# Kernel tuning notes

Hardware: AMD Instinct MI355X
Metric: run time of the kernel (lower is better)

Reference implementation:

```python
import jax, jax.numpy as jnp
import numpy as np

H = 64
VOCAB = 128
LN_EPS = 1e-5
NORM_EPS = 1e-12


def _l2norm(k):
    # F.normalize(..., dim=-1): x / max(||x||_2, eps)
    n = jnp.sqrt(jnp.sum(k * k, axis=-1, keepdims=True))
    return k / jnp.maximum(n, NORM_EPS)


def _delta_scan(M0, ks, vs):
    # ks, vs: [L, B, H] time-major; M0: [B, H, H]
    def step(M, kv):
        k, v = kv
        Mk = jnp.einsum('bij,bj->bi', M, k)            # [B,H]
        M = M + (v - Mk)[:, :, None] * k[:, None, :]   # rank-1 update
        return M, None
    M, _ = jax.lax.scan(step, M0, (ks, vs))
    return M


def reference(x, embed, W1, b1, W2, b2, ln_g, ln_b, Wk, Wv, Wq, Wattn, Wout, bout):
    # Encoder: embed -> residual FF -> LayerNorm
    h = embed[x]                                        # [B,L,H]
    ff = jnp.maximum(h @ W1.T + b1, 0.0) @ W2.T + b2
    z = h + ff
    mu = jnp.mean(z, axis=-1, keepdims=True)
    var = jnp.mean((z - mu) ** 2, axis=-1, keepdims=True)
    hidden = (z - mu) / jnp.sqrt(var + LN_EPS) * ln_g + ln_b  # [B,L,H]

    B, L, _ = hidden.shape
    # First delta-rule memory write over all L steps
    ks = _l2norm(hidden @ Wk.T)                         # [B,L,H]
    vs = hidden @ Wv.T                                  # [B,L,H]
    M0 = jnp.zeros((B, H, H), dtype=hidden.dtype)
    M = _delta_scan(M0, jnp.swapaxes(ks, 0, 1), jnp.swapaxes(vs, 0, 1))

    half = L // 2
    slots = jnp.swapaxes(M, 1, 2)                       # [B,H,H] = M^T
    q = hidden[:, :half, :] @ Wattn.T                   # [B,half,H]
    # bmm(q, slots^T) = q @ M
    attn = jax.nn.softmax(jnp.einsum('bth,bhk->btk', q, M) / jnp.sqrt(jnp.asarray(H, hidden.dtype)), axis=-1)
    ctx = jnp.einsum('btk,bkh->bth', attn, slots)       # [B,half,H]

    # Second delta-rule write seeded from M
    ks2 = _l2norm(ctx @ Wk.T)
    vs2 = ctx @ Wv.T
    M2 = _delta_scan(M, jnp.swapaxes(ks2, 0, 1), jnp.swapaxes(vs2, 0, 1))

    q_last = hidden[:, -1, :] @ Wq.T                    # [B,H]
    read = jnp.einsum('bij,bj->bi', M2, q_last)         # [B,H]
    return read @ Wout.T + bout                         # [B,VOCAB]


def setup_inputs() -> dict:
    key = jax.random.key(0)
    ks = jax.random.split(key, 16)
    B, L = 64, 4096
    s = 0.05
    return {
        'x': jax.random.randint(ks[0], (B, L), 0, VOCAB),
        'embed': jax.random.normal(ks[1], (VOCAB, H), jnp.float32) * s,
        'W1': jax.random.normal(ks[2], (2 * H, H), jnp.float32) * s,
        'b1': jnp.zeros((2 * H,), jnp.float32),
        'W2': jax.random.normal(ks[3], (H, 2 * H), jnp.float32) * s,
        'b2': jnp.zeros((H,), jnp.float32),
        'ln_g': jnp.ones((H,), jnp.float32),
        'ln_b': jnp.zeros((H,), jnp.float32),
        'Wk': jax.random.normal(ks[4], (H, H), jnp.float32) * s,
        'Wv': jax.random.normal(ks[5], (H, H), jnp.float32) * s,
        'Wq': jax.random.normal(ks[6], (H, H), jnp.float32) * s,
        'Wattn': jax.random.normal(ks[7], (H, H), jnp.float32) * s,
        'Wout': jax.random.normal(ks[8], (VOCAB, H), jnp.float32) * s,
        'bout': jnp.zeros((VOCAB,), jnp.float32),
    }
```

## Files before the change

### kernel.cpp

```cpp
#include <hip/hip_runtime.h>

#define SEQL 4096
#define NB 64

__device__ __forceinline__ float dpp_xor1_add(float x) {
    int v = __builtin_amdgcn_mov_dpp(__float_as_int(x), 0xB1, 0xF, 0xF, true);
    return x + __int_as_float(v);
}
__device__ __forceinline__ float dpp_xor2_add(float x) {
    int v = __builtin_amdgcn_mov_dpp(__float_as_int(x), 0x4E, 0xF, 0xF, true);
    return x + __int_as_float(v);
}

#define FMA16(A, W, H)                                      \
    A[0]  = fmaf(W.x, H.x, A[0]);  A[1]  = fmaf(W.x, H.y, A[1]);   \
    A[2]  = fmaf(W.x, H.z, A[2]);  A[3]  = fmaf(W.x, H.w, A[3]);   \
    A[4]  = fmaf(W.y, H.x, A[4]);  A[5]  = fmaf(W.y, H.y, A[5]);   \
    A[6]  = fmaf(W.y, H.z, A[6]);  A[7]  = fmaf(W.y, H.w, A[7]);   \
    A[8]  = fmaf(W.z, H.x, A[8]);  A[9]  = fmaf(W.z, H.y, A[9]);   \
    A[10] = fmaf(W.z, H.z, A[10]); A[11] = fmaf(W.z, H.w, A[11]);  \
    A[12] = fmaf(W.w, H.x, A[12]); A[13] = fmaf(W.w, H.y, A[13]);  \
    A[14] = fmaf(W.w, H.z, A[14]); A[15] = fmaf(W.w, H.w, A[15])

__device__ __forceinline__ void proj_tile64(const float* __restrict__ sW,
                                            const float* __restrict__ sA,
                                            int jq, int tq, float* __restrict__ a)
{
#pragma unroll
    for (int u = 0; u < 16; ++u) a[u] = 0.f;
#pragma unroll 4
    for (int i = 0; i < 64; ++i) {
        float4 w  = *reinterpret_cast<const float4*>(&sW[i * 68 + jq]);
        float4 h4 = *reinterpret_cast<const float4*>(&sA[i * 68 + tq]);
        FMA16(a, w, h4);
    }
}

__device__ __forceinline__ void load_w_t(const float* __restrict__ W, int ldw, int col0,
                                         int tid, float4* __restrict__ r)
{
    const int j = tid & 63;
    const int cq0 = tid >> 6;
#pragma unroll
    for (int it = 0; it < 4; ++it)
        r[it] = *reinterpret_cast<const float4*>(&W[(size_t)j * ldw + col0 + (it * 4 + cq0) * 4]);
}
__device__ __forceinline__ void write_w_t(const float4* __restrict__ r,
                                          float* __restrict__ sWb, int tid)
{
    const int j = tid & 63;
    const int cq0 = tid >> 6;
#pragma unroll
    for (int it = 0; it < 4; ++it) {
        const int c = (it * 4 + cq0) * 4;
        sWb[(c + 0) * 68 + j] = r[it].x;
        sWb[(c + 1) * 68 + j] = r[it].y;
        sWb[(c + 2) * 68 + j] = r[it].z;
        sWb[(c + 3) * 68 + j] = r[it].w;
    }
}

__device__ __forceinline__ void stage_w_t(const float* __restrict__ W, int ldw, int col0,
                                          float* __restrict__ sWb, int tid)
{
    float4 r[4];
    load_w_t(W, ldw, col0, tid, r);
    write_w_t(r, sWb, tid);
}
__device__ __forceinline__ void stage_w_n(const float* __restrict__ W,
                                          float* __restrict__ sWb, int tid)
{
#pragma unroll
    for (int it = 0; it < 4; ++it) {
        int item = it * 256 + tid;
        int r = item >> 4, c4 = item & 15;
        float4 w = *reinterpret_cast<const float4*>(&W[(size_t)r * 64 + c4 * 4]);
        *reinterpret_cast<float4*>(&sWb[r * 68 + c4 * 4]) = w;
    }
}

__global__ __launch_bounds__(256) void encoder_kernel(
    const int* __restrict__ x, const float* __restrict__ embed,
    const float* __restrict__ W1, const float* __restrict__ b1,
    const float* __restrict__ W2, const float* __restrict__ b2,
    const float* __restrict__ ln_g, const float* __restrict__ ln_b,
    const float* __restrict__ Wk, const float* __restrict__ Wv,
    const float* __restrict__ Wq, const float* __restrict__ Wattn,
    float* __restrict__ ks, float* __restrict__ vs,
    float* __restrict__ qbuf, float* __restrict__ qlast)
{
    __shared__ __align__(16) float sZ[64 * 68];
    __shared__ __align__(16) float sF[64 * 68];
    __shared__ __align__(16) float sW[64 * 68];

    const int tid = threadIdx.x;
    const size_t g0 = (size_t)blockIdx.x * 64;
    const int b = (int)(g0 >> 12);
    const int l0 = (int)(g0 & (SEQL - 1));
    const int jq = (tid & 15) * 4;
    const int tq = (tid >> 4) * 4;
    const bool doq = (l0 < 2048);
    const bool dolast = (l0 == SEQL - 64);

    float4 pf[4], pf2[4];

    load_w_t(W1, 64, 0, tid, pf);
    for (int idx = tid; idx < 4096; idx += 256) {
        int t = idx >> 6, i = idx & 63;
        sZ[i * 68 + t] = embed[(size_t)x[g0 + t] * 64 + i];
    }
    write_w_t(pf, sW, tid);
    load_w_t(W2, 128, 0, tid, pf2);
    __syncthreads();

    float zacc[16];
#pragma unroll
    for (int u = 0; u < 16; ++u) zacc[u] = 0.f;

    {
        float a[16];
        proj_tile64(sW, sZ, jq, tq, a);
        float4 bb = *reinterpret_cast<const float4*>(&b1[jq]);
        float bv[4] = {bb.x, bb.y, bb.z, bb.w};
#pragma unroll
        for (int u = 0; u < 4; ++u) {
            float4 o;
            o.x = fmaxf(a[u * 4 + 0] + bv[u], 0.f);
            o.y = fmaxf(a[u * 4 + 1] + bv[u], 0.f);
            o.z = fmaxf(a[u * 4 + 2] + bv[u], 0.f);
            o.w = fmaxf(a[u * 4 + 3] + bv[u], 0.f);
            *reinterpret_cast<float4*>(&sF[(jq + u) * 68 + tq]) = o;
        }
    }
    __syncthreads();
    write_w_t(pf2, sW, tid);
    load_w_t(W1 + 4096, 64, 0, tid, pf);
    __syncthreads();
#pragma unroll 4
    for (int p = 0; p < 64; ++p) {
        float4 w  = *reinterpret_cast<const float4*>(&sW[p * 68 + jq]);
        float4 f4 = *reinterpret_cast<const float4*>(&sF[p * 68 + tq]);
        FMA16(zacc, w, f4);
    }
    __syncthreads();
    write_w_t(pf, sW, tid);
    load_w_t(W2, 128, 64, tid, pf2);
    __syncthreads();
    {
        float a[16];
        proj_tile64(sW, sZ, jq, tq, a);
        float4 bb = *reinterpret_cast<const float4*>(&b1[64 + jq]);
        float bv[4] = {bb.x, bb.y, bb.z, bb.w};
#pragma unroll
        for (int u = 0; u < 4; ++u) {
            float4 o;
            o.x = fmaxf(a[u * 4 + 0] + bv[u], 0.f);
            o.y = fmaxf(a[u * 4 + 1] + bv[u], 0.f);
            o.z = fmaxf(a[u * 4 + 2] + bv[u], 0.f);
            o.w = fmaxf(a[u * 4 + 3] + bv[u], 0.f);
            *reinterpret_cast<float4*>(&sF[(jq + u) * 68 + tq]) = o;
        }
    }
    __syncthreads();
    write_w_t(pf2, sW, tid);
    load_w_t(Wk, 64, 0, tid, pf);
    load_w_t(Wv, 64, 0, tid, pf2);
    __syncthreads();
#pragma unroll 4
    for (int p = 0; p < 64; ++p) {
        float4 w  = *reinterpret_cast<const float4*>(&sW[p * 68 + jq]);
        float4 f4 = *reinterpret_cast<const float4*>(&sF[p * 68 + tq]);
        FMA16(zacc, w, f4);
    }

    {
        float z[16];
        float4 b2v = *reinterpret_cast<const float4*>(&b2[jq]);
        float bv[4] = {b2v.x, b2v.y, b2v.z, b2v.w};
#pragma unroll
        for (int u = 0; u < 4; ++u) {
            float4 h4 = *reinterpret_cast<const float4*>(&sZ[(jq + u) * 68 + tq]);
            z[u * 4 + 0] = h4.x + bv[u] + zacc[u * 4 + 0];
            z[u * 4 + 1] = h4.y + bv[u] + zacc[u * 4 + 1];
            z[u * 4 + 2] = h4.z + bv[u] + zacc[u * 4 + 2];
            z[u * 4 + 3] = h4.w + bv[u] + zacc[u * 4 + 3];
        }
        float s[4], ss[4];
#pragma unroll
        for (int v = 0; v < 4; ++v) {
            s[v]  = z[v] + z[4 + v] + z[8 + v] + z[12 + v];
            ss[v] = z[v] * z[v] + z[4 + v] * z[4 + v]
                  + z[8 + v] * z[8 + v] + z[12 + v] * z[12 + v];
        }
#pragma unroll
        for (int m = 1; m <= 8; m <<= 1) {
#pragma unroll
            for (int v = 0; v < 4; ++v) {
                s[v]  += __shfl_xor(s[v], m);
                ss[v] += __shfl_xor(ss[v], m);
            }
        }
        float mu[4], inv[4];
#pragma unroll
        for (int v = 0; v < 4; ++v) {
            mu[v] = s[v] * 0.015625f;
            float var = ss[v] * 0.015625f - mu[v] * mu[v];
            inv[v] = rsqrtf(var + 1e-5f);
        }
        float4 g4  = *reinterpret_cast<const float4*>(&ln_g[jq]);
        float4 be4 = *reinterpret_cast<const float4*>(&ln_b[jq]);
        float gv[4] = {g4.x, g4.y, g4.z, g4.w};
        float bev[4] = {be4.x, be4.y, be4.z, be4.w};
#pragma unroll
        for (int u = 0; u < 4; ++u) {
            float4 o;
            o.x = (z[u * 4 + 0] - mu[0]) * inv[0] * gv[u] + bev[u];
            o.y = (z[u * 4 + 1] - mu[1]) * inv[1] * gv[u] + bev[u];
            o.z = (z[u * 4 + 2] - mu[2]) * inv[2] * gv[u] + bev[u];
            o.w = (z[u * 4 + 3] - mu[3]) * inv[3] * gv[u] + bev[u];
            *reinterpret_cast<float4*>(&sZ[(jq + u) * 68 + tq]) = o;
        }
    }
    __syncthreads();
    write_w_t(pf, sW, tid);
    write_w_t(pf2, sF, tid);
    if (doq)        load_w_t(Wattn, 64, 0, tid, pf);
    else if (dolast) load_w_t(Wq, 64, 0, tid, pf);
    __syncthreads();

    {
        float a[16];
        proj_tile64(sW, sZ, jq, tq, a);
        float ssq[4];
#pragma unroll
        for (int v = 0; v < 4; ++v)
            ssq[v] = a[v] * a[v] + a[4 + v] * a[4 + v]
                   + a[8 + v] * a[8 + v] + a[12 + v] * a[12 + v];
#pragma unroll
        for (int m = 1; m <= 8; m <<= 1) {
#pragma unroll
            for (int v = 0; v < 4; ++v) ssq[v] += __shfl_xor(ssq[v], m);
        }
#pragma unroll
        for (int v = 0; v < 4; ++v) {
            float sc = 1.f / fmaxf(sqrtf(ssq[v]), 1e-12f);
            float4 o = make_float4(a[v] * sc, a[4 + v] * sc, a[8 + v] * sc, a[12 + v] * sc);
            *reinterpret_cast<float4*>(&ks[(g0 + tq + v) * 64 + jq]) = o;
        }
    }
    {
        float a[16];
        proj_tile64(sF, sZ, jq, tq, a);
#pragma unroll
        for (int v = 0; v < 4; ++v) {
            float4 o = make_float4(a[v], a[4 + v], a[8 + v], a[12 + v]);
            *reinterpret_cast<float4*>(&vs[(g0 + tq + v) * 64 + jq]) = o;
        }
    }

    if (doq || dolast) {
        __syncthreads();
        write_w_t(pf, sW, tid);
        __syncthreads();
        float a[16];
        proj_tile64(sW, sZ, jq, tq, a);
        if (doq) {
#pragma unroll
            for (int v = 0; v < 4; ++v) {
                float4 o = make_float4(a[v], a[4 + v], a[8 + v], a[12 + v]);
                *reinterpret_cast<float4*>(&qbuf[((size_t)b * 2048 + l0 + tq + v) * 64 + jq]) = o;
            }
        } else if ((tid >> 4) == 15) {
            float4 o = make_float4(a[3], a[7], a[11], a[15]);
            *reinterpret_cast<float4*>(&qlast[(size_t)b * 64 + jq]) = o;
        }
    }
}

#define STEP2(K0, K1, K2, K3, V)                                                \
    do {                                                                        \
        float dp0 = fmaf(p[0], K0.x, fmaf(p[1], K0.y, fmaf(p[2], K0.z, p[3] * K0.w))); \
        float dp1 = fmaf(p[4], K1.x, fmaf(p[5], K1.y, fmaf(p[6], K1.z, p[7] * K1.w))); \
        float dp2 = fmaf(p[8], K2.x, fmaf(p[9], K2.y, fmaf(p[10], K2.z, p[11] * K2.w))); \
        float dp3 = fmaf(p[12], K3.x, fmaf(p[13], K3.y, fmaf(p[14], K3.z, p[15] * K3.w))); \
        float dq0 = fmaf(q[0], K0.x, fmaf(q[1], K0.y, fmaf(q[2], K0.z, q[3] * K0.w))); \
        float dq1 = fmaf(q[4], K1.x, fmaf(q[5], K1.y, fmaf(q[6], K1.z, q[7] * K1.w))); \
        float dq2 = fmaf(q[8], K2.x, fmaf(q[9], K2.y, fmaf(q[10], K2.z, q[11] * K2.w))); \
        float dq3 = fmaf(q[12], K3.x, fmaf(q[13], K3.y, fmaf(q[14], K3.z, q[15] * K3.w))); \
        float ddp = (dp0 + dp1) + (dp2 + dp3);                                  \
        float ddq = (dq0 + dq1) + (dq2 + dq3);                                  \
        ddp = dpp_xor1_add(ddp);  ddq = dpp_xor1_add(ddq);                      \
        ddp = dpp_xor2_add(ddp);  ddq = dpp_xor2_add(ddq);                      \
        float up = -ddp;                                                        \
        float uq = V - ddq;                                                     \
        p[0] = fmaf(up, K0.x, p[0]);   q[0] = fmaf(uq, K0.x, q[0]);             \
        p[1] = fmaf(up, K0.y, p[1]);   q[1] = fmaf(uq, K0.y, q[1]);             \
        p[2] = fmaf(up, K0.z, p[2]);   q[2] = fmaf(uq, K0.z, q[2]);             \
        p[3] = fmaf(up, K0.w, p[3]);   q[3] = fmaf(uq, K0.w, q[3]);             \
        p[4] = fmaf(up, K1.x, p[4]);   q[4] = fmaf(uq, K1.x, q[4]);             \
        p[5] = fmaf(up, K1.y, p[5]);   q[5] = fmaf(uq, K1.y, q[5]);             \
        p[6] = fmaf(up, K1.z, p[6]);   q[6] = fmaf(uq, K1.z, q[6]);             \
        p[7] = fmaf(up, K1.w, p[7]);   q[7] = fmaf(uq, K1.w, q[7]);             \
        p[8] = fmaf(up, K2.x, p[8]);   q[8] = fmaf(uq, K2.x, q[8]);             \
        p[9] = fmaf(up, K2.y, p[9]);   q[9] = fmaf(uq, K2.y, q[9]);             \
        p[10] = fmaf(up, K2.z, p[10]); q[10] = fmaf(uq, K2.z, q[10]);           \
        p[11] = fmaf(up, K2.w, p[11]); q[11] = fmaf(uq, K2.w, q[11]);           \
        p[12] = fmaf(up, K3.x, p[12]); q[12] = fmaf(uq, K3.x, q[12]);           \
        p[13] = fmaf(up, K3.y, p[13]); q[13] = fmaf(uq, K3.y, q[13]);           \
        p[14] = fmaf(up, K3.z, p[14]); q[14] = fmaf(uq, K3.z, q[14]);           \
        p[15] = fmaf(up, K3.w, p[15]); q[15] = fmaf(uq, K3.w, q[15]);           \
    } while (0)

__global__ __launch_bounds__(256) void chunk_kernel(
    float* __restrict__ ksb, float* __restrict__ vsb, int C)
{
    __shared__ __align__(16) float sk[2][32 * 64];
    __shared__ __align__(16) float sv[2][32 * 64];

    const int job = blockIdx.x;
    const int tid = threadIdx.x;
    const int r = tid >> 2;
    const int c0 = (tid & 3) * 16;
    float* kc = ksb + (size_t)job * C * 64;
    float* vc = vsb + (size_t)job * C * 64;

    float p[16], q[16];
#pragma unroll
    for (int j = 0; j < 16; ++j) { p[j] = (c0 + j == r) ? 1.f : 0.f; q[j] = 0.f; }

    const int nt = C >> 5;
    float4 rk0, rk1, rv0, rv1;

    {
        const float4* gk = reinterpret_cast<const float4*>(kc);
        const float4* gv = reinterpret_cast<const float4*>(vc);
        float4 a0 = gk[tid], a1 = gk[256 + tid];
        float4 b0 = gv[tid], b1 = gv[256 + tid];
        float4* dk = reinterpret_cast<float4*>(sk[0]);
        float4* dv = reinterpret_cast<float4*>(sv[0]);
        dk[tid] = a0; dk[256 + tid] = a1;
        dv[tid] = b0; dv[256 + tid] = b1;
    }
    if (nt > 1) {
        const float4* gk = reinterpret_cast<const float4*>(kc + 2048);
        const float4* gv = reinterpret_cast<const float4*>(vc + 2048);
        rk0 = gk[tid]; rk1 = gk[256 + tid];
        rv0 = gv[tid]; rv1 = gv[256 + tid];
    }
    __syncthreads();

    int cur = 0;
    for (int tile = 0; tile < nt; ++tile) {
        if (tile + 1 < nt) {
            float4* dk = reinterpret_cast<float4*>(sk[cur ^ 1]);
            float4* dv = reinterpret_cast<float4*>(sv[cur ^ 1]);
            dk[tid] = rk0; dk[256 + tid] = rk1;
            dv[tid] = rv0; dv[256 + tid] = rv1;
            if (tile + 2 < nt) {
                const float4* gk = reinterpret_cast<const float4*>(kc + (size_t)(tile + 2) * 2048);
                const float4* gv = reinterpret_cast<const float4*>(vc + (size_t)(tile + 2) * 2048);
                rk0 = gk[tid]; rk1 = gk[256 + tid];
                rv0 = gv[tid]; rv1 = gv[256 + tid];
            }
        }

        const float* kl = sk[cur] + c0;
        const float* vl = sv[cur] + r;
        float4 a0, a1, a2, a3, e0, e1, e2, e3;
        float va, ve;
        {
            const float4* kp = reinterpret_cast<const float4*>(kl);
            a0 = kp[0]; a1 = kp[1]; a2 = kp[2]; a3 = kp[3];
            va = vl[0];
        }
#pragma unroll
        for (int t = 0; t < 32; t += 2) {
            {
                const float4* kp = reinterpret_cast<const float4*>(kl + (t + 1) * 64);
                e0 = kp[0]; e1 = kp[1]; e2 = kp[2]; e3 = kp[3];
                ve = vl[(t + 1) * 64];
            }
            STEP2(a0, a1, a2, a3, va);
            if (t + 2 < 32) {
                const float4* kp = reinterpret_cast<const float4*>(kl + (t + 2) * 64);
                a0 = kp[0]; a1 = kp[1]; a2 = kp[2]; a3 = kp[3];
                va = vl[(t + 2) * 64];
            }
            STEP2(e0, e1, e2, e3, ve);
        }
        __syncthreads();
        cur ^= 1;
    }

    float4* po = reinterpret_cast<float4*>(kc + r * 64 + c0);
    po[0] = make_float4(p[0], p[1], p[2], p[3]);
    po[1] = make_float4(p[4], p[5], p[6], p[7]);
    po[2] = make_float4(p[8], p[9], p[10], p[11]);
    po[3] = make_float4(p[12], p[13], p[14], p[15]);
    float4* qo = reinterpret_cast<float4*>(vc + r * 64 + c0);
    qo[0] = make_float4(q[0], q[1], q[2], q[3]);
    qo[1] = make_float4(q[4], q[5], q[6], q[7]);
    qo[2] = make_float4(q[8], q[9], q[10], q[11]);
    qo[3] = make_float4(q[12], q[13], q[14], q[15]);
}

__global__ __launch_bounds__(256) void combine_kernel(
    const float* __restrict__ Pb, const float* __restrict__ Qb,
    const float* __restrict__ Min, float* __restrict__ Mout,
    int nc, int chunk_stride)
{
    __shared__ __align__(16) float sP[2][64 * 64];
    __shared__ __align__(16) float sM[2][16 * 68];
    const int bb = blockIdx.x;
    const int b = bb >> 2;
    const int r0 = (bb & 3) << 4;
    const int tid = threadIdx.x;
    const int rl = tid >> 4;
    const int j4 = (tid & 15) * 4;
    const int gr = r0 + rl;

    if (Min) {
        *reinterpret_cast<float4*>(&sM[0][rl * 68 + j4]) =
            *reinterpret_cast<const float4*>(Min + ((size_t)b * 64 + gr) * 64 + j4);
    } else {
        *reinterpret_cast<float4*>(&sM[0][rl * 68 + j4]) = make_float4(0.f, 0.f, 0.f, 0.f);
    }
    {
        const float4* g = reinterpret_cast<const float4*>(Pb + (size_t)b * nc * chunk_stride);
        float4* s = reinterpret_cast<float4*>(sP[0]);
        for (int i = tid; i < 1024; i += 256) s[i] = g[i];
    }
    __syncthreads();

    int cur = 0;
    for (int c = 0; c < nc; ++c) {
        const size_t cbase = (size_t)(b * nc + c) * chunk_stride;
        float4 rp0, rp1, rp2, rp3;
        if (c + 1 < nc) {
            const float4* g = reinterpret_cast<const float4*>(Pb + cbase + chunk_stride);
            rp0 = g[tid]; rp1 = g[tid + 256]; rp2 = g[tid + 512]; rp3 = g[tid + 768];
        }
        float4 rq = *reinterpret_cast<const float4*>(Qb + cbase + (size_t)gr * 64 + j4);

        float ax = 0.f, ay = 0.f, az = 0.f, aw = 0.f;
        const float* Mrow = &sM[cur][rl * 68];
        const float* Pl = sP[c & 1];
#pragma unroll 4
        for (int mg = 0; mg < 16; ++mg) {
            float4 a4 = *reinterpret_cast<const float4*>(Mrow + mg * 4);
            float4 p0 = *reinterpret_cast<const float4*>(Pl + (mg * 4 + 0) * 64 + j4);
            float4 p1 = *reinterpret_cast<const float4*>(Pl + (mg * 4 + 1) * 64 + j4);
            float4 p2 = *reinterpret_cast<const float4*>(Pl + (mg * 4 + 2) * 64 + j4);
            float4 p3 = *reinterpret_cast<const float4*>(Pl + (mg * 4 + 3) * 64 + j4);
            ax = fmaf(a4.x, p0.x, ax); ay = fmaf(a4.x, p0.y, ay);
            az = fmaf(a4.x, p0.z, az); aw = fmaf(a4.x, p0.w, aw);
            ax = fmaf(a4.y, p1.x, ax); ay = fmaf(a4.y, p1.y, ay);
            az = fmaf(a4.y, p1.z, az); aw = fmaf(a4.y, p1.w, aw);
            ax = fmaf(a4.z, p2.x, ax); ay = fmaf(a4.z, p2.y, ay);
            az = fmaf(a4.z, p2.z, az); aw = fmaf(a4.z, p2.w, aw);
            ax = fmaf(a4.w, p3.x, ax); ay = fmaf(a4.w, p3.y, ay);
            az = fmaf(a4.w, p3.z, az); aw = fmaf(a4.w, p3.w, aw);
        }
        const int nxt = cur ^ 1;
        *reinterpret_cast<float4*>(&sM[nxt][rl * 68 + j4]) =
            make_float4(ax + rq.x, ay + rq.y, az + rq.z, aw + rq.w);
        if (c + 1 < nc) {
            float4* s = reinterpret_cast<float4*>(sP[(c + 1) & 1]);
            s[tid] = rp0; s[tid + 256] = rp1; s[tid + 512] = rp2; s[tid + 768] = rp3;
        }
        __syncthreads();
        cur = nxt;
    }
    *reinterpret_cast<float4*>(Mout + ((size_t)b * 64 + gr) * 64 + j4) =
        *reinterpret_cast<const float4*>(&sM[cur][rl * 68 + j4]);
}

__global__ __launch_bounds__(256) void attn_kernel(
    const float* __restrict__ qg, const float* __restrict__ Mbuf,
    const float* __restrict__ Wk, const float* __restrict__ Wv,
    float* __restrict__ ks2, float* __restrict__ vs2)
{
    __shared__ __align__(16) float sW1[64 * 68];
    __shared__ __align__(16) float sW2[64 * 68];
    __shared__ __align__(16) float sA[64 * 68];
    __shared__ __align__(16) float sB[64 * 68];

    const int b = blockIdx.y;
    const int tile0 = blockIdx.x * 64;
    const int tid = threadIdx.x;
    const int jq = (tid & 15) * 4;
    const int tq = (tid >> 4) * 4;
    const size_t qbase = (size_t)b * 2048 + tile0;
    const float* Mb = Mbuf + (size_t)b * 4096;

    stage_w_n(Mb, sW1, tid);
    stage_w_t(Mb, 64, 0, sW2, tid);
    stage_w_t(qg + qbase * 64, 64, 0, sA, tid);
    __syncthreads();

    float a[16];
    proj_tile64(sW1, sA, jq, tq, a);
#pragma unroll
    for (int u = 0; u < 16; ++u) a[u] *= 0.125f;

    {
        float mx[4], sm[4];
#pragma unroll
        for (int v = 0; v < 4; ++v)
            mx[v] = fmaxf(fmaxf(a[v], a[4 + v]), fmaxf(a[8 + v], a[12 + v]));
#pragma unroll
        for (int m = 1; m <= 8; m <<= 1) {
#pragma unroll
            for (int v = 0; v < 4; ++v) mx[v] = fmaxf(mx[v], __shfl_xor(mx[v], m));
        }
#pragma unroll
        for (int v = 0; v < 4; ++v) {
            a[v]      = __expf(a[v]      - mx[v]);
            a[4 + v]  = __expf(a[4 + v]  - mx[v]);
            a[8 + v]  = __expf(a[8 + v]  - mx[v]);
            a[12 + v] = __expf(a[12 + v] - mx[v]);
            sm[v] = a[v] + a[4 + v] + a[8 + v] + a[12 + v];
        }
#pragma unroll
        for (int m = 1; m <= 8; m <<= 1) {
#pragma unroll
            for (int v = 0; v < 4; ++v) sm[v] += __shfl_xor(sm[v], m);
        }
        float rinv[4];
#pragma unroll
        for (int v = 0; v < 4; ++v) rinv[v] = 1.f / sm[v];
#pragma unroll
        for (int v = 0; v < 4; ++v) {
            a[v] *= rinv[v]; a[4 + v] *= rinv[v];
            a[8 + v] *= rinv[v]; a[12 + v] *= rinv[v];
        }
    }
#pragma unroll
    for (int u = 0; u < 4; ++u)
        *reinterpret_cast<float4*>(&sB[(jq + u) * 68 + tq]) =
            make_float4(a[u * 4 + 0], a[u * 4 + 1], a[u * 4 + 2], a[u * 4 + 3]);
    __syncthreads();

    float c[16];
    proj_tile64(sW2, sB, jq, tq, c);
#pragma unroll
    for (int u = 0; u < 4; ++u)
        *reinterpret_cast<float4*>(&sA[(jq + u) * 68 + tq]) =
            make_float4(c[u * 4 + 0], c[u * 4 + 1], c[u * 4 + 2], c[u * 4 + 3]);
    __syncthreads();

    stage_w_t(Wk, 64, 0, sW1, tid);
    stage_w_t(Wv, 64, 0, sW2, tid);
    __syncthreads();

    float ak[16], av[16];
#pragma unroll
    for (int u = 0; u < 16; ++u) { ak[u] = 0.f; av[u] = 0.f; }
#pragma unroll 2
    for (int i = 0; i < 64; ++i) {
        float4 wk = *reinterpret_cast<const float4*>(&sW1[i * 68 + jq]);
        float4 wv = *reinterpret_cast<const float4*>(&sW2[i * 68 + jq]);
        float4 c4 = *reinterpret_cast<const float4*>(&sA[i * 68 + tq]);
        FMA16(ak, wk, c4);
        FMA16(av, wv, c4);
    }

    {
        float ssq[4];
#pragma unroll
        for (int v = 0; v < 4; ++v)
            ssq[v] = ak[v] * ak[v] + ak[4 + v] * ak[4 + v]
                   + ak[8 + v] * ak[8 + v] + ak[12 + v] * ak[12 + v];
#pragma unroll
        for (int m = 1; m <= 8; m <<= 1) {
#pragma unroll
            for (int v = 0; v < 4; ++v) ssq[v] += __shfl_xor(ssq[v], m);
        }
#pragma unroll
        for (int v = 0; v < 4; ++v) {
            float sc = 1.f / fmaxf(sqrtf(ssq[v]), 1e-12f);
            const size_t o = (qbase + tq + v) * 64 + jq;
            *reinterpret_cast<float4*>(&ks2[o]) =
                make_float4(ak[v] * sc, ak[4 + v] * sc, ak[8 + v] * sc, ak[12 + v] * sc);
            *reinterpret_cast<float4*>(&vs2[o]) =
                make_float4(av[v], av[4 + v], av[8 + v], av[12 + v]);
        }
    }
}

__global__ __launch_bounds__(128) void out_kernel(
    const float* __restrict__ M2, const float* __restrict__ qlast,
    const float* __restrict__ Wout, const float* __restrict__ bout,
    float* __restrict__ out)
{
    const int b = blockIdx.x;
    const int tid = threadIdx.x;
    __shared__ float sq[64], sread[64];
    if (tid < 64) sq[tid] = qlast[b * 64 + tid];
    __syncthreads();
    if (tid < 64) {
        const float* Mr = M2 + ((size_t)b * 64 + tid) * 64;
        float acc = 0.f;
        for (int j = 0; j < 64; ++j) acc = fmaf(Mr[j], sq[j], acc);
        sread[tid] = acc;
    }
    __syncthreads();
    float acc = bout[tid];
    for (int h = 0; h < 64; ++h) acc = fmaf(Wout[tid * 64 + h], sread[h], acc);
    out[b * 128 + tid] = acc;
}

extern "C" void kernel_launch(void* const* d_in, const int* in_sizes, int n_in,
                              void* d_out, int out_size, void* d_ws, size_t ws_size,
                              hipStream_t stream)
{
    const int* x        = (const int*)d_in[0];
    const float* embed  = (const float*)d_in[1];
    const float* W1     = (const float*)d_in[2];
    const float* b1     = (const float*)d_in[3];
    const float* W2     = (const float*)d_in[4];
    const float* b2     = (const float*)d_in[5];
    const float* ln_g   = (const float*)d_in[6];
    const float* ln_b   = (const float*)d_in[7];
    const float* Wk     = (const float*)d_in[8];
    const float* Wv     = (const float*)d_in[9];
    const float* Wq     = (const float*)d_in[10];
    const float* Wattn  = (const float*)d_in[11];
    const float* Wout   = (const float*)d_in[12];
    const float* bout   = (const float*)d_in[13];

    float* ws = (float*)d_ws;
    float* ks = ws;
    float* vs = ks + (size_t)NB * SEQL * 64;
    float* qb = vs + (size_t)NB * SEQL * 64;
    float* ql = qb + (size_t)NB * 2048 * 64;
    float* M  = ql + (size_t)NB * 64;
    float* M2 = M + (size_t)NB * 64 * 64;
    if (ws_size < (size_t)(M2 + (size_t)NB * 64 * 64 - ws) * sizeof(float)) return;

    hipLaunchKernelGGL(encoder_kernel, dim3((NB * SEQL) / 64), dim3(256), 0, stream,
                       x, embed, W1, b1, W2, b2, ln_g, ln_b, Wk, Wv, Wq, Wattn,
                       ks, vs, qb, ql);

    const int C1 = 256, nc1 = SEQL / C1;
    hipLaunchKernelGGL(chunk_kernel, dim3(NB * nc1), dim3(256), 0, stream, ks, vs, C1);
    hipLaunchKernelGGL(combine_kernel, dim3(NB * 4), dim3(256), 0, stream,
                       ks, vs, (const float*)nullptr, M, nc1, C1 * 64);

    hipLaunchKernelGGL(attn_kernel, dim3(32, NB), dim3(256), 0, stream,
                       qb, M, Wk, Wv, ks, vs);

    const int C2 = 128, nc2 = 2048 / C2;
    hipLaunchKernelGGL(chunk_kernel, dim3(NB * nc2), dim3(256), 0, stream, ks, vs, C2);
    hipLaunchKernelGGL(combine_kernel, dim3(NB * 4), dim3(256), 0, stream,
                       ks, vs, M, M2, nc2, C2 * 64);

    hipLaunchKernelGGL(out_kernel, dim3(NB), dim3(128), 0, stream,
                       M2, ql, Wout, bout, (float*)d_out);
}
```

Baseline: 494.6 us.

## Fold Wattn, Wk, Wv into per-batch memory matrices before attention

A new per-batch precompute kernel forms Wattn-times-M, M-times-Wk^T and M-times-Wv^T once, so the attention kernel reads the hidden states directly instead of a separately projected q buffer. The encoder now writes the first half of the hidden states transposed instead of computing the Wattn projection. The attention kernel drops one 64x64 matmul stage per tile along with its shared buffer and barrier, and prefetches MK through registers. In exchange it adds a small extra launch and roughly 64K extra floats of workspace reads, and it changes the floating-point association order.

```diff
diff --git a/kernel.cpp b/kernel.cpp
--- a/kernel.cpp
+++ b/kernel.cpp
@@ -85,9 +85,9 @@
     const float* __restrict__ W2, const float* __restrict__ b2,
     const float* __restrict__ ln_g, const float* __restrict__ ln_b,
     const float* __restrict__ Wk, const float* __restrict__ Wv,
-    const float* __restrict__ Wq, const float* __restrict__ Wattn,
+    const float* __restrict__ Wq,
     float* __restrict__ ks, float* __restrict__ vs,
-    float* __restrict__ qbuf, float* __restrict__ qlast)
+    float* __restrict__ hidT, float* __restrict__ qlast)
 {
     __shared__ __align__(16) float sZ[64 * 68];
     __shared__ __align__(16) float sF[64 * 68];
@@ -224,8 +224,7 @@
     __syncthreads();
     write_w_t(pf, sW, tid);
     write_w_t(pf2, sF, tid);
-    if (doq)        load_w_t(Wattn, 64, 0, tid, pf);
-    else if (dolast) load_w_t(Wq, 64, 0, tid, pf);
+    if (dolast) load_w_t(Wq, 64, 0, tid, pf);
     __syncthreads();
 
     {
@@ -258,22 +257,74 @@
         }
     }
 
-    if (doq || dolast) {
+    if (doq) {
+#pragma unroll
+        for (int it = 0; it < 4; ++it) {
+            int item = it * 256 + tid;
+            int i = item >> 4, q4 = (item & 15) * 4;
+            float4 v = *reinterpret_cast<const float4*>(&sZ[i * 68 + q4]);
+            *reinterpret_cast<float4*>(&hidT[((size_t)b * 64 + i) * 2048 + l0 + q4]) = v;
+        }
+    }
+
+    if (dolast) {
         __syncthreads();
         write_w_t(pf, sW, tid);
         __syncthreads();
         float a[16];
         proj_tile64(sW, sZ, jq, tq, a);
-        if (doq) {
-#pragma unroll
-            for (int v = 0; v < 4; ++v) {
-                float4 o = make_float4(a[v], a[4 + v], a[8 + v], a[12 + v]);
-                *reinterpret_cast<float4*>(&qbuf[((size_t)b * 2048 + l0 + tq + v) * 64 + jq]) = o;
-            }
-        } else if ((tid >> 4) == 15) {
+        if ((tid >> 4) == 15) {
             float4 o = make_float4(a[3], a[7], a[11], a[15]);
             *reinterpret_cast<float4*>(&qlast[(size_t)b * 64 + jq]) = o;
         }
+    }
+}
+
+__global__ __launch_bounds__(256) void precompute_kernel(
+    const float* __restrict__ Mbuf, const float* __restrict__ Wattn,
+    const float* __restrict__ Wk, const float* __restrict__ Wv,
+    float* __restrict__ WAM, float* __restrict__ MK, float* __restrict__ MV)
+{
+    __shared__ __align__(16) float sM[64 * 68];
+    __shared__ __align__(16) float sOp[64 * 68];
+    const int b = blockIdx.x;
+    const int tid = threadIdx.x;
+    const int jq = (tid & 15) * 4;
+    const int tq = (tid >> 4) * 4;
+    const float* Mb = Mbuf + (size_t)b * 4096;
+
+    stage_w_n(Mb, sM, tid);
+    stage_w_n(Wattn, sOp, tid);
+    __syncthreads();
+    {
+        float a[16];
+        proj_tile64(sM, sOp, jq, tq, a);
+#pragma unroll
+        for (int v = 0; v < 4; ++v)
+            *reinterpret_cast<float4*>(&WAM[(size_t)b * 4096 + (tq + v) * 64 + jq]) =
+                make_float4(a[v], a[4 + v], a[8 + v], a[12 + v]);
+    }
+    __syncthreads();
+    stage_w_t(Wk, 64, 0, sOp, tid);
+    __syncthreads();
+    {
+        float a[16];
+        proj_tile64(sM, sOp, jq, tq, a);
+#pragma unroll
+        for (int v = 0; v < 4; ++v)
+            *reinterpret_cast<float4*>(&MK[(size_t)b * 4096 + (tq + v) * 64 + jq]) =
+                make_float4(a[v], a[4 + v], a[8 + v], a[12 + v]);
+    }
+    __syncthreads();
+    stage_w_t(Wv, 64, 0, sOp, tid);
+    __syncthreads();
+    {
+        float a[16];
+        proj_tile64(sM, sOp, jq, tq, a);
+#pragma unroll
+        for (int v = 0; v < 4; ++v)
+            *reinterpret_cast<float4*>(&MV[(size_t)b * 4096 + (tq + v) * 64 + jq]) =
+                make_float4(a[v], a[4 + v], a[8 + v], a[12 + v]);
     }
 }
 
@@ -476,14 +527,13 @@
 }
 
 __global__ __launch_bounds__(256) void attn_kernel(
-    const float* __restrict__ qg, const float* __restrict__ Mbuf,
-    const float* __restrict__ Wk, const float* __restrict__ Wv,
+    const float* __restrict__ hidT, const float* __restrict__ WAM,
+    const float* __restrict__ MK, const float* __restrict__ MV,
     float* __restrict__ ks2, float* __restrict__ vs2)
 {
     __shared__ __align__(16) float sW1[64 * 68];
     __shared__ __align__(16) float sW2[64 * 68];
     __shared__ __align__(16) float sA[64 * 68];
-    __shared__ __align__(16) float sB[64 * 68];
 
     const int b = blockIdx.y;
     const int tile0 = blockIdx.x * 64;
@@ -491,11 +541,19 @@
     const int jq = (tid & 15) * 4;
     const int tq = (tid >> 4) * 4;
     const size_t qbase = (size_t)b * 2048 + tile0;
-    const float* Mb = Mbuf + (size_t)b * 4096;
-
-    stage_w_n(Mb, sW1, tid);
-    stage_w_t(Mb, 64, 0, sW2, tid);
-    stage_w_t(qg + qbase * 64, 64, 0, sA, tid);
+    const float* hb = hidT + (size_t)b * 64 * 2048 + tile0;
+
+    float4 pfk[4];
+    stage_w_n(WAM + (size_t)b * 4096, sW1, tid);
+    stage_w_t(MV + (size_t)b * 4096, 64, 0, sW2, tid);
+#pragma unroll
+    for (int it = 0; it < 4; ++it) {
+        int item = it * 256 + tid;
+        int i = item >> 4, q4 = (item & 15) * 4;
+        float4 v = *reinterpret_cast<const float4*>(&hb[(size_t)i * 2048 + q4]);
+        *reinterpret_cast<float4*>(&sA[i * 68 + q4]) = v;
+    }
+    load_w_t(MK + (size_t)b * 4096, 64, 0, tid, pfk);
     __syncthreads();
 
     float a[16];
@@ -535,22 +593,12 @@
             a[8 + v] *= rinv[v]; a[12 + v] *= rinv[v];
         }
     }
-#pragma unroll
-    for (int u = 0; u < 4; ++u)
-        *reinterpret_cast<float4*>(&sB[(jq + u) * 68 + tq]) =
-            make_float4(a[u * 4 + 0], a[u * 4 + 1], a[u * 4 + 2], a[u * 4 + 3]);
-    __syncthreads();
-
-    float c[16];
-    proj_tile64(sW2, sB, jq, tq, c);
+    __syncthreads();
 #pragma unroll
     for (int u = 0; u < 4; ++u)
         *reinterpret_cast<float4*>(&sA[(jq + u) * 68 + tq]) =
-            make_float4(c[u * 4 + 0], c[u * 4 + 1], c[u * 4 + 2], c[u * 4 + 3]);
-    __syncthreads();
-
-    stage_w_t(Wk, 64, 0, sW1, tid);
-    stage_w_t(Wv, 64, 0, sW2, tid);
+            make_float4(a[u * 4 + 0], a[u * 4 + 1], a[u * 4 + 2], a[u * 4 + 3]);
+    write_w_t(pfk, sW1, tid);
     __syncthreads();
 
     float ak[16], av[16];
@@ -560,9 +608,9 @@
     for (int i = 0; i < 64; ++i) {
         float4 wk = *reinterpret_cast<const float4*>(&sW1[i * 68 + jq]);
         float4 wv = *reinterpret_cast<const float4*>(&sW2[i * 68 + jq]);
-        float4 c4 = *reinterpret_cast<const float4*>(&sA[i * 68 + tq]);
-        FMA16(ak, wk, c4);
-        FMA16(av, wv, c4);
+        float4 p4 = *reinterpret_cast<const float4*>(&sA[i * 68 + tq]);
+        FMA16(ak, wk, p4);
+        FMA16(av, wv, p4);
     }
 
     {
@@ -630,25 +678,31 @@
     const float* bout   = (const float*)d_in[13];
 
     float* ws = (float*)d_ws;
-    float* ks = ws;
-    float* vs = ks + (size_t)NB * SEQL * 64;
-    float* qb = vs + (size_t)NB * SEQL * 64;
-    float* ql = qb + (size_t)NB * 2048 * 64;
-    float* M  = ql + (size_t)NB * 64;
-    float* M2 = M + (size_t)NB * 64 * 64;
-    if (ws_size < (size_t)(M2 + (size_t)NB * 64 * 64 - ws) * sizeof(float)) return;
+    float* ks  = ws;
+    float* vs  = ks  + (size_t)NB * SEQL * 64;
+    float* hid = vs  + (size_t)NB * SEQL * 64;
+    float* ql  = hid + (size_t)NB * 2048 * 64;
+    float* M   = ql  + (size_t)NB * 64;
+    float* M2  = M   + (size_t)NB * 64 * 64;
+    float* WAM = M2  + (size_t)NB * 64 * 64;
+    float* MK  = WAM + (size_t)NB * 64 * 64;
+    float* MV  = MK  + (size_t)NB * 64 * 64;
+    if (ws_size < (size_t)(MV + (size_t)NB * 64 * 64 - ws) * sizeof(float)) return;
 
     hipLaunchKernelGGL(encoder_kernel, dim3((NB * SEQL) / 64), dim3(256), 0, stream,
-                       x, embed, W1, b1, W2, b2, ln_g, ln_b, Wk, Wv, Wq, Wattn,
-                       ks, vs, qb, ql);
+                       x, embed, W1, b1, W2, b2, ln_g, ln_b, Wk, Wv, Wq,
+                       ks, vs, hid, ql);
 
     const int C1 = 256, nc1 = SEQL / C1;
     hipLaunchKernelGGL(chunk_kernel, dim3(NB * nc1), dim3(256), 0, stream, ks, vs, C1);
     hipLaunchKernelGGL(combine_kernel, dim3(NB * 4), dim3(256), 0, stream,
                        ks, vs, (const float*)nullptr, M, nc1, C1 * 64);
 
+    hipLaunchKernelGGL(precompute_kernel, dim3(NB), dim3(256), 0, stream,
+                       M, Wattn, Wk, Wv, WAM, MK, MV);
+
     hipLaunchKernelGGL(attn_kernel, dim3(32, NB), dim3(256), 0, stream,
-                       qb, M, Wk, Wv, ks, vs);
+                       hid, WAM, MK, MV, ks, vs);
 
     const int C2 = 128, nc2 = 2048 / C2;
     hipLaunchKernelGGL(chunk_kernel, dim3(NB * nc2), dim3(256), 0, stream, ks, vs, C2);
```

Measured after the change: 474.5 us, median of 2. 1.04x faster.
